# Kernel optimization log

Measured on AMD Instinct MI355X. Metric: run time of the kernel, lower is better.

## Reference

```python
import jax, jax.numpy as jnp
import numpy as np

H = 8          # num heads
DK = 64        # d_model // H
D_MODEL = 512
WIN = 256


def setup_inputs() -> dict:
    key = jax.random.key(0)
    ks = jax.random.split(key, 12)
    B, S = 2, 2048
    mk = lambda k, shape, s=1.0: jax.random.normal(k, shape, dtype=jnp.float32) * s
    inp = {
        "query": mk(ks[0], (B, S, D_MODEL)),
        "key_in": mk(ks[1], (B, S, D_MODEL)),
        "value": mk(ks[2], (B, S, D_MODEL)),
        # nn.Linear(d_model, d_model) weights (out,in) and biases, x4
        "Wq": mk(ks[3], (D_MODEL, D_MODEL), 0.02), "bq": jnp.zeros((D_MODEL,), jnp.float32),
        "Wk": mk(ks[4], (D_MODEL, D_MODEL), 0.02), "bk": jnp.zeros((D_MODEL,), jnp.float32),
        "Wv": mk(ks[5], (D_MODEL, D_MODEL), 0.02), "bv": jnp.zeros((D_MODEL,), jnp.float32),
        "Wo": mk(ks[6], (D_MODEL, D_MODEL), 0.02), "bo": jnp.zeros((D_MODEL,), jnp.float32),
    }
    return inp


def reference(query, key_in, value, Wq, bq, Wk, bk, Wv, bv, Wo, bo):
    B, S, D = query.shape
    scale = np.float32(1.0 / np.sqrt(DK))

    def proj(x, W, b):
        # (B,S,D) -> (B,H,S,DK)
        return (x @ W.T + b).reshape(B, S, H, DK).transpose(0, 2, 1, 3)

    q = proj(query, Wq, bq)
    k = proj(key_in, Wk, bk)
    v = proj(value, Wv, bv)

    # Faithful to naive_masked_matmul: full (B,H,S,S) scores, with entries
    # OUTSIDE the sliding window left at exactly 0.0 (NOT -inf) before softmax.
    scores = jnp.einsum('bhid,bhjd->bhij', q, k) * scale
    idx = jnp.arange(S)
    band = jnp.abs(idx[:, None] - idx[None, :]) <= (WIN // 2)  # (S,S) bool
    scores = jnp.where(band, scores, jnp.float32(0.0))

    p_attn = jax.nn.softmax(scores, axis=-1)
    x = jnp.einsum('bhij,bhjd->bhid', p_attn, v)          # (B,H,S,DK)
    x = x.transpose(0, 2, 1, 3).reshape(B, S, D)          # (B,S,D)
    return x @ Wo.T + bo
```

## Files before the change

kernel.cpp:

```cpp
#include <hip/hip_runtime.h>
#include <hip/hip_bf16.h>

#define SS 2048
#define DD 512
#define HWIN 128

typedef __bf16 bf16x8 __attribute__((ext_vector_type(8)));
typedef unsigned short u16x8 __attribute__((ext_vector_type(8)));
typedef float f32x4 __attribute__((ext_vector_type(4)));

__device__ __forceinline__ unsigned short f2bf(float x) {
    unsigned u = __builtin_bit_cast(unsigned, x);
    return (unsigned short)((u + 0x7fffu + ((u >> 16) & 1u)) >> 16);
}
__device__ __forceinline__ float bf2f(unsigned short s) {
    unsigned u = ((unsigned)s) << 16;
    return __builtin_bit_cast(float, u);
}
__device__ __forceinline__ void split_bf(float x, unsigned short& h, unsigned short& l) {
    h = f2bf(x);
    l = f2bf(x - bf2f(h));
}
__device__ __forceinline__ f32x4 mfma16(u16x8 a, u16x8 b, f32x4 c) {
    return __builtin_amdgcn_mfma_f32_16x16x32_bf16(
        __builtin_bit_cast(bf16x8, a), __builtin_bit_cast(bf16x8, b), c, 0, 0, 0);
}
__device__ __forceinline__ void gload16(const unsigned short* g, unsigned short* l) {
    __builtin_amdgcn_global_load_lds(
        (const __attribute__((address_space(1))) unsigned int*)g,
        (__attribute__((address_space(3))) unsigned int*)l, 16, 0, 0);
}

__global__ __launch_bounds__(256) void castAll(
    const float* __restrict__ q, const float* __restrict__ k, const float* __restrict__ v,
    const float* __restrict__ wq, const float* __restrict__ wk,
    const float* __restrict__ wv, const float* __restrict__ wo,
    unsigned short* __restrict__ QAh, unsigned short* __restrict__ KAh,
    unsigned short* __restrict__ VAh,
    unsigned short* __restrict__ WQh, unsigned short* __restrict__ WKh,
    unsigned short* __restrict__ WVh, unsigned short* __restrict__ WoP)
{
    const size_t e0 = ((size_t)blockIdx.x * 256 + threadIdx.x) * 8;
    const float* src; size_t off; unsigned short* dsth; bool paired = false;
    if      (e0 < 2097152) { src = q; off = e0;           dsth = QAh + off; }
    else if (e0 < 4194304) { src = k; off = e0 - 2097152; dsth = KAh + off; }
    else if (e0 < 6291456) { src = v; off = e0 - 4194304; dsth = VAh + off; }
    else {
        const size_t e = e0 - 6291456;
        if      (e < 262144) { src = wq; off = e;          dsth = WQh + off; }
        else if (e < 524288) { src = wk; off = e - 262144; dsth = WKh + off; }
        else if (e < 786432) { src = wv; off = e - 524288; dsth = WVh + off; }
        else { src = wo; off = e - 786432; dsth = WoP + 2 * (e - 786432); paired = true; }
    }
    const float4 f0 = *(const float4*)(src + off), f1 = *(const float4*)(src + off + 4);
    const float vals[8] = {f0.x, f0.y, f0.z, f0.w, f1.x, f1.y, f1.z, f1.w};
    u16x8 h;
    #pragma unroll
    for (int i = 0; i < 8; ++i) h[i] = f2bf(vals[i]);
    *(u16x8*)dsth = h;
    if (paired) {
        u16x8 l;
        #pragma unroll
        for (int i = 0; i < 8; ++i) l[i] = f2bf(vals[i] - bf2f(h[i]));
        *(u16x8*)(dsth + 8) = l;
    }
}

__global__ __launch_bounds__(256) void proj_gemm(
    const unsigned short* __restrict__ QAh, const unsigned short* __restrict__ KAh,
    const unsigned short* __restrict__ VAh,
    const unsigned short* __restrict__ WQh, const unsigned short* __restrict__ WKh,
    const unsigned short* __restrict__ WVh,
    const float* __restrict__ bq, const float* __restrict__ bk, const float* __restrict__ bv,
    unsigned short* __restrict__ base,
    unsigned short* __restrict__ VTH, float* __restrict__ part)
{
    const int d = blockIdx.x;
    const int hi = d >> 6, low = d & 63;
    const int x = low >> 3, rsw = low & 7;
    const int g = hi * 8 + rsw;
    const int y = g / 3, z = g - y * 3;

    const unsigned short* Ap = (z == 0) ? QAh : ((z == 1) ? KAh : VAh);
    const unsigned short* Wp = (z == 0) ? WQh : ((z == 1) ? WKh : WVh);
    const float* bias = (z == 0) ? bq : ((z == 1) ? bk : bv);
    unsigned short* OH = base + (size_t)z * 4194304;

    const int m0 = y * 128, n0 = x * 64;

    __shared__ unsigned short Ah[16 * 64 * 8];
    __shared__ unsigned short Bh[8 * 64 * 8];

    const int tid = threadIdx.x, wave = tid >> 6, lane = tid & 63;
    const int lm = lane & 15, lq = lane >> 4;
    const int wm = wave >> 1, wn = wave & 1;
    const int kb = lq * 8;

    f32x4 acc[4][2] = {};

    const int ar0 = m0 + (wave * 2 + 0) * 16 + lm;
    const int ar1 = m0 + (wave * 2 + 1) * 16 + lm;
    const int br  = n0 + wave * 16 + lm;

    const int aoff0 = ((wave * 2 + 0) * 64 + lane) * 8;
    const int aoff1 = ((wave * 2 + 1) * 64 + lane) * 8;
    const int boff  = (wave * 64 + lane) * 8;

    for (int k0 = 0; k0 < 512; k0 += 64) {
        __syncthreads();
        gload16(Ap + (size_t)ar0 * 512 + k0 + kb,      &Ah[aoff0]);
        gload16(Ap + (size_t)ar1 * 512 + k0 + kb,      &Ah[aoff1]);
        gload16(Wp + (size_t)br  * 512 + k0 + kb,      &Bh[boff]);
        gload16(Ap + (size_t)ar0 * 512 + k0 + 32 + kb, &Ah[4096 + aoff0]);
        gload16(Ap + (size_t)ar1 * 512 + k0 + 32 + kb, &Ah[4096 + aoff1]);
        gload16(Wp + (size_t)br  * 512 + k0 + 32 + kb, &Bh[2048 + boff]);
        __syncthreads();

        #pragma unroll
        for (int s = 0; s < 2; ++s) {
            u16x8 afh[4], bfh[2];
            #pragma unroll
            for (int i = 0; i < 4; ++i)
                afh[i] = *(const u16x8*)&Ah[s * 4096 + ((wm * 4 + i) * 64 + lane) * 8];
            #pragma unroll
            for (int j = 0; j < 2; ++j)
                bfh[j] = *(const u16x8*)&Bh[s * 2048 + ((wn * 2 + j) * 64 + lane) * 8];
            #pragma unroll
            for (int i = 0; i < 4; ++i)
                #pragma unroll
                for (int j = 0; j < 2; ++j)
                    acc[i][j] = mfma16(afh[i], bfh[j], acc[i][j]);
        }
    }

    if (z < 2) {
        #pragma unroll
        for (int i = 0; i < 4; ++i)
            #pragma unroll
            for (int j = 0; j < 2; ++j) {
                const int col = n0 + (wn * 2 + j) * 16 + lm;
                const float bv_ = bias[col];
                #pragma unroll
                for (int r = 0; r < 4; ++r) {
                    const int row = m0 + (wm * 4 + i) * 16 + lq * 4 + r;
                    OH[(size_t)row * 512 + col] = f2bf(acc[i][j][r] + bv_);
                }
            }
    } else {
        float csum[2] = {0.f, 0.f};
        #pragma unroll
        for (int i = 0; i < 4; ++i)
            #pragma unroll
            for (int j = 0; j < 2; ++j) {
                const int col = n0 + (wn * 2 + j) * 16 + lm;
                const float bv_ = bias[col];
                #pragma unroll
                for (int r = 0; r < 4; ++r) {
                    const int row = m0 + (wm * 4 + i) * 16 + lq * 4 + r;
                    const float vv = acc[i][j][r] + bv_;
                    csum[j] += vv;
                    const size_t vix =
                        (((size_t)(row >> 11) * 8 + (col >> 6)) * 64 + (col & 63)) * 2048
                        + (row & 2047);
                    VTH[vix] = f2bf(vv);
                }
            }
        #pragma unroll
        for (int j = 0; j < 2; ++j) {
            float s = csum[j];
            s += __shfl_xor(s, 16);
            s += __shfl_xor(s, 32);
            if (lq == 0) {
                const int col = n0 + (wn * 2 + j) * 16 + lm;
                part[(size_t)(y * 2 + wm) * 512 + col] = s;
            }
        }
    }
}

__global__ __launch_bounds__(256) void out_gemm(
    const unsigned short* __restrict__ XHg,
    const unsigned short* __restrict__ WoP, const float* __restrict__ bo,
    float* __restrict__ O)
{
    const int gid = blockIdx.x;
    const int rr = gid & 7, hi = gid >> 3;
    const int nblk = hi & 7, mhi = hi >> 3;
    const int mblk = mhi * 8 + rr;
    const int m0 = mblk * 64, n0 = nblk * 64;

    __shared__ unsigned short Ah[2 * 4096];
    __shared__ unsigned short Bh[2 * 4096], Bl[2 * 4096];

    const int tid = threadIdx.x, wave = tid >> 6, lane = tid & 63;
    const int lm = lane & 15, lq = lane >> 4;
    const int kb = lq * 8;

    f32x4 acc[4] = {};

    const int arow = m0 + wave * 16 + lm;
    const int brow = n0 + wave * 16 + lm;

    #define OSTAGE(k0_, bs)                                                     \
    {                                                                           \
        _Pragma("unroll")                                                       \
        for (int s = 0; s < 2; ++s) {                                           \
            const int o = (bs) * 4096 + ((s * 4 + wave) * 64 + lane) * 8;       \
            gload16(XHg + (size_t)arow * 512 + (k0_) + s * 32 + kb, &Ah[o]);    \
            const unsigned short* pw =                                          \
                WoP + 2 * ((size_t)brow * 512 + (k0_) + s * 32 + kb);           \
            gload16(pw,     &Bh[o]);                                            \
            gload16(pw + 8, &Bl[o]);                                            \
        }                                                                       \
    }

    OSTAGE(0, 0);
    __syncthreads();

    for (int t = 0; t < 8; ++t) {
        const int cur = t & 1;
        if (t < 7) OSTAGE((t + 1) * 64, cur ^ 1);

        #pragma unroll
        for (int s = 0; s < 2; ++s) {
            const u16x8 a_h = *(const u16x8*)&Ah[cur * 4096 + ((s * 4 + wave) * 64 + lane) * 8];
            #pragma unroll
            for (int j = 0; j < 4; ++j) {
                const u16x8 b_h = *(const u16x8*)&Bh[cur * 4096 + ((s * 4 + j) * 64 + lane) * 8];
                const u16x8 b_l = *(const u16x8*)&Bl[cur * 4096 + ((s * 4 + j) * 64 + lane) * 8];
                acc[j] = mfma16(a_h, b_h, acc[j]);
                acc[j] = mfma16(a_h, b_l, acc[j]);
            }
        }

        __syncthreads();
    }
    #undef OSTAGE

    #pragma unroll
    for (int j = 0; j < 4; ++j) {
        const int col = n0 + j * 16 + lm;
        const float bv_ = bo[col];
        #pragma unroll
        for (int r = 0; r < 4; ++r) {
            const int row = m0 + wave * 16 + lq * 4 + r;
            O[(size_t)row * 512 + col] = acc[j][r] + bv_;
        }
    }
}

__global__ __launch_bounds__(256) void attn_mfma(
    const unsigned short* __restrict__ QH, const unsigned short* __restrict__ KH,
    const unsigned short* __restrict__ VTH, const float* __restrict__ part,
    unsigned short* __restrict__ XH)
{
    const int dblk = blockIdx.x;
    const int bhi = dblk >> 8, blow = dblk & 255;
    const int xblk = blow >> 3, rrs = blow & 7;
    const int bh = bhi * 8 + rrs;
    const int h = bh & 7, b = bh >> 3;
    const int i0 = xblk * 64;
    const int tid = threadIdx.x, wave = tid >> 6, lane = tid & 63;
    const int lm = lane & 15, lq = lane >> 4;
    const int kb = lq * 8;

    __shared__ unsigned short KfH[2 * 8 * 64 * 8];
    __shared__ unsigned short VfH[2 * 8 * 64 * 8];
    __shared__ unsigned short Swh[64][72];

    const size_t qoff = ((size_t)(b * SS + i0 + wave * 16 + lm)) * DD + h * 64 + kb;
    const u16x8 aQ0h = *(const u16x8*)(QH + qoff);
    const u16x8 aQ1h = *(const u16x8*)(QH + qoff + 32);

    f32x4 oacc[4] = {};
    float dacc[4] = {0.f, 0.f, 0.f, 0.f};

    const size_t vrow = ((size_t)bh * 64 + wave * 16 + lm) * 2048;
    const int s0 = (wave * 2 + 0) * 64 * 8 + lane * 8;
    const int s1 = (wave * 2 + 1) * 64 * 8 + lane * 8;

    #define STAGE(jt_, bufsel)                                                  \
    {                                                                           \
        const int jt0_ = i0 - 128 + (jt_) * 64;                                 \
        const int jrow = jt0_ + wave * 16 + lm;                                 \
        const int jrc = min(max(jrow, 0), SS - 1);                              \
        const size_t kgb = ((size_t)(b * SS + jrc)) * DD + h * 64 + kb;         \
        gload16(KH + kgb,      &KfH[(bufsel) * 4096 + s0]);                     \
        gload16(KH + kgb + 32, &KfH[(bufsel) * 4096 + s1]);                     \
        const int j0c = min(max(jt0_ + kb, 0), SS - 8);                         \
        const int j1c = min(max(jt0_ + 32 + kb, 0), SS - 8);                    \
        gload16(VTH + vrow + j0c, &VfH[(bufsel) * 4096 + s0]);                  \
        gload16(VTH + vrow + j1c, &VfH[(bufsel) * 4096 + s1]);                  \
    }

    STAGE(0, 0);
    __syncthreads();

    for (int jt = 0; jt < 5; ++jt) {
        const int buf = jt & 1;
        if (jt < 4) STAGE(jt + 1, buf ^ 1);
        const int jt0 = i0 - 128 + jt * 64;
        const int rmin = i0 + wave * 16;

        #pragma unroll
        for (int js = 0; js < 4; ++js) {
            const int j0 = js * 16;
            const int cmin = jt0 + j0, cmax = cmin + 15;
            const bool skip = (cmax < 0) || (cmin >= SS) ||
                              (cmax < rmin - HWIN) || (cmin > rmin + 15 + HWIN);
            if (skip) {
                #pragma unroll
                for (int r = 0; r < 4; ++r)
                    Swh[wave * 16 + lq * 4 + r][j0 + lm] = 0;
                continue;
            }
            const u16x8 bK0h = *(const u16x8*)&KfH[buf * 4096 + ((js * 2 + 0) * 64 + lane) * 8];
            const u16x8 bK1h = *(const u16x8*)&KfH[buf * 4096 + ((js * 2 + 1) * 64 + lane) * 8];
            f32x4 s = {0.f, 0.f, 0.f, 0.f};
            s = mfma16(aQ0h, bK0h, s);
            s = mfma16(aQ1h, bK1h, s);
            const int jg = jt0 + j0 + lm;
            const int iq = i0 + wave * 16 + lq * 4;
            #pragma unroll
            for (int r = 0; r < 4; ++r) {
                const int qi = iq + r;
                const bool in = ((unsigned)jg < (unsigned)SS) &&
                                ((unsigned)(jg - qi + HWIN) <= (unsigned)(2 * HWIN));
                const float w = in ? (__expf(s[r] * 0.125f) - 1.0f) : 0.0f;
                dacc[r] += w;
                Swh[wave * 16 + lq * 4 + r][j0 + lm] = f2bf(w);
            }
        }

        const u16x8 aP0h = *(const u16x8*)&Swh[wave * 16 + lm][kb];
        const u16x8 aP1h = *(const u16x8*)&Swh[wave * 16 + lm][kb + 32];
        #pragma unroll
        for (int s4 = 0; s4 < 4; ++s4) {
            const u16x8 bV0h = *(const u16x8*)&VfH[buf * 4096 + ((s4 * 2 + 0) * 64 + lane) * 8];
            const u16x8 bV1h = *(const u16x8*)&VfH[buf * 4096 + ((s4 * 2 + 1) * 64 + lane) * 8];
            oacc[s4] = mfma16(aP0h, bV0h, oacc[s4]);
            oacc[s4] = mfma16(aP1h, bV1h, oacc[s4]);
        }
        __syncthreads();
    }
    #undef STAGE

    #pragma unroll
    for (int r = 0; r < 4; ++r) {
        float v = dacc[r];
        v += __shfl_xor(v, 1);
        v += __shfl_xor(v, 2);
        v += __shfl_xor(v, 4);
        v += __shfl_xor(v, 8);
        dacc[r] = v + 2048.0f;
    }

    #pragma unroll
    for (int s4 = 0; s4 < 4; ++s4) {
        const float* pp = part + (size_t)(b * 32) * 512 + h * 64 + s4 * 16 + lm;
        float vsv = 0.f;
        #pragma unroll 8
        for (int p = 0; p < 32; ++p) vsv += pp[(size_t)p * 512];
        #pragma unroll
        for (int r = 0; r < 4; ++r) {
            const int qrow = i0 + wave * 16 + lq * 4 + r;
            const float x = (oacc[s4][r] + vsv) / dacc[r];
            const size_t ix = ((size_t)(b * SS + qrow)) * DD + h * 64 + s4 * 16 + lm;
            XH[ix] = f2bf(x);
        }
    }
}

extern "C" void kernel_launch(void* const* d_in, const int* in_sizes, int n_in,
                              void* d_out, int out_size, void* d_ws, size_t ws_size,
                              hipStream_t stream)
{
    const float* query  = (const float*)d_in[0];
    const float* key_in = (const float*)d_in[1];
    const float* value  = (const float*)d_in[2];
    const float* Wq = (const float*)d_in[3]; const float* bq = (const float*)d_in[4];
    const float* Wk = (const float*)d_in[5]; const float* bk = (const float*)d_in[6];
    const float* Wv = (const float*)d_in[7]; const float* bv = (const float*)d_in[8];
    const float* Wo = (const float*)d_in[9]; const float* bo = (const float*)d_in[10];

    unsigned short* wsb = (unsigned short*)d_ws;
    unsigned short* QH  = wsb;
    unsigned short* KH  = wsb + 4194304;
    unsigned short* VTH = wsb + 8388608;
    unsigned short* XH  = wsb + 12582912;
    unsigned short* WQh = wsb + 16777216;
    unsigned short* WKh = wsb + 17039360;
    unsigned short* WVh = wsb + 17301504;
    unsigned short* WoP = wsb + 17825792;
    unsigned short* QAh = wsb + 18350080;
    unsigned short* KAh = wsb + 20447232;
    unsigned short* VAh = wsb + 22544384;
    float* partp = (float*)((char*)d_ws + 63045632);

    castAll<<<3584, 256, 0, stream>>>(query, key_in, value, Wq, Wk, Wv, Wo,
                                      QAh, KAh, VAh, WQh, WKh, WVh, WoP);

    proj_gemm<<<768, 256, 0, stream>>>(QAh, KAh, VAh, WQh, WKh, WVh,
                                       bq, bk, bv, QH, VTH, partp);

    attn_mfma<<<512, 256, 0, stream>>>(QH, KH, VTH, partp, XH);

    out_gemm<<<512, 256, 0, stream>>>(XH, WoP, bo, (float*)d_out);
}
```

Before: 144.9 us.

## Give each wave private LDS staging to drop block barriers in projection and attention

Both the QKV projection GEMM and the windowed attention kernel now have each wave load its own fragments into a per-wave LDS region and wait with s_waitcnt vmcnt(0), instead of cooperatively staging shared tiles between __syncthreads. This removes block-wide barriers and, in attention, the double-buffered prefetch. The cost is redundant global/L2 traffic, since waves reload the same B and K/V tiles, plus more LDS per block and no overlap of loads with compute. Keeping the Swh writes and reads consistent within a wave without the barrier relies on per-wave row ownership.

```diff
diff --git a/kernel.cpp b/kernel.cpp
--- a/kernel.cpp
+++ b/kernel.cpp
@@ -8,6 +8,8 @@
 typedef __bf16 bf16x8 __attribute__((ext_vector_type(8)));
 typedef unsigned short u16x8 __attribute__((ext_vector_type(8)));
 typedef float f32x4 __attribute__((ext_vector_type(4)));
+
+#define VMCNT0() asm volatile("s_waitcnt vmcnt(0)" ::: "memory")
 
 __device__ __forceinline__ unsigned short f2bf(float x) {
     unsigned u = __builtin_bit_cast(unsigned, x);
@@ -88,8 +90,8 @@
 
     const int m0 = y * 128, n0 = x * 64;
 
-    __shared__ unsigned short Ah[16 * 64 * 8];
-    __shared__ unsigned short Bh[8 * 64 * 8];
+    __shared__ unsigned short Aw[4][8][512];
+    __shared__ unsigned short Bw[4][4][512];
 
     const int tid = threadIdx.x, wave = tid >> 6, lane = tid & 63;
     const int lm = lane & 15, lq = lane >> 4;
@@ -98,33 +100,35 @@
 
     f32x4 acc[4][2] = {};
 
-    const int ar0 = m0 + (wave * 2 + 0) * 16 + lm;
-    const int ar1 = m0 + (wave * 2 + 1) * 16 + lm;
-    const int br  = n0 + wave * 16 + lm;
-
-    const int aoff0 = ((wave * 2 + 0) * 64 + lane) * 8;
-    const int aoff1 = ((wave * 2 + 1) * 64 + lane) * 8;
-    const int boff  = (wave * 64 + lane) * 8;
+    size_t arow[4], brow[2];
+    #pragma unroll
+    for (int i = 0; i < 4; ++i)
+        arow[i] = (size_t)(m0 + (wm * 4 + i) * 16 + lm) * 512;
+    #pragma unroll
+    for (int j = 0; j < 2; ++j)
+        brow[j] = (size_t)(n0 + (wn * 2 + j) * 16 + lm) * 512;
 
     for (int k0 = 0; k0 < 512; k0 += 64) {
-        __syncthreads();
-        gload16(Ap + (size_t)ar0 * 512 + k0 + kb,      &Ah[aoff0]);
-        gload16(Ap + (size_t)ar1 * 512 + k0 + kb,      &Ah[aoff1]);
-        gload16(Wp + (size_t)br  * 512 + k0 + kb,      &Bh[boff]);
-        gload16(Ap + (size_t)ar0 * 512 + k0 + 32 + kb, &Ah[4096 + aoff0]);
-        gload16(Ap + (size_t)ar1 * 512 + k0 + 32 + kb, &Ah[4096 + aoff1]);
-        gload16(Wp + (size_t)br  * 512 + k0 + 32 + kb, &Bh[2048 + boff]);
-        __syncthreads();
+        #pragma unroll
+        for (int s = 0; s < 2; ++s) {
+            #pragma unroll
+            for (int i = 0; i < 4; ++i)
+                gload16(Ap + arow[i] + k0 + s * 32 + kb, &Aw[wave][s * 4 + i][lane * 8]);
+            #pragma unroll
+            for (int j = 0; j < 2; ++j)
+                gload16(Wp + brow[j] + k0 + s * 32 + kb, &Bw[wave][s * 2 + j][lane * 8]);
+        }
+        VMCNT0();
 
         #pragma unroll
         for (int s = 0; s < 2; ++s) {
             u16x8 afh[4], bfh[2];
             #pragma unroll
             for (int i = 0; i < 4; ++i)
-                afh[i] = *(const u16x8*)&Ah[s * 4096 + ((wm * 4 + i) * 64 + lane) * 8];
+                afh[i] = *(const u16x8*)&Aw[wave][s * 4 + i][lane * 8];
             #pragma unroll
             for (int j = 0; j < 2; ++j)
-                bfh[j] = *(const u16x8*)&Bh[s * 2048 + ((wn * 2 + j) * 64 + lane) * 8];
+                bfh[j] = *(const u16x8*)&Bw[wave][s * 2 + j][lane * 8];
             #pragma unroll
             for (int i = 0; i < 4; ++i)
                 #pragma unroll
@@ -264,8 +268,8 @@
     const int lm = lane & 15, lq = lane >> 4;
     const int kb = lq * 8;
 
-    __shared__ unsigned short KfH[2 * 8 * 64 * 8];
-    __shared__ unsigned short VfH[2 * 8 * 64 * 8];
+    __shared__ unsigned short Kw[4][8][512];
+    __shared__ unsigned short Vw[4][8][512];
     __shared__ unsigned short Swh[64][72];
 
     const size_t qoff = ((size_t)(b * SS + i0 + wave * 16 + lm)) * DD + h * 64 + kb;
@@ -275,31 +279,27 @@
     f32x4 oacc[4] = {};
     float dacc[4] = {0.f, 0.f, 0.f, 0.f};
 
-    const size_t vrow = ((size_t)bh * 64 + wave * 16 + lm) * 2048;
-    const int s0 = (wave * 2 + 0) * 64 * 8 + lane * 8;
-    const int s1 = (wave * 2 + 1) * 64 * 8 + lane * 8;
-
-    #define STAGE(jt_, bufsel)                                                  \
-    {                                                                           \
-        const int jt0_ = i0 - 128 + (jt_) * 64;                                 \
-        const int jrow = jt0_ + wave * 16 + lm;                                 \
-        const int jrc = min(max(jrow, 0), SS - 1);                              \
-        const size_t kgb = ((size_t)(b * SS + jrc)) * DD + h * 64 + kb;         \
-        gload16(KH + kgb,      &KfH[(bufsel) * 4096 + s0]);                     \
-        gload16(KH + kgb + 32, &KfH[(bufsel) * 4096 + s1]);                     \
-        const int j0c = min(max(jt0_ + kb, 0), SS - 8);                         \
-        const int j1c = min(max(jt0_ + 32 + kb, 0), SS - 8);                    \
-        gload16(VTH + vrow + j0c, &VfH[(bufsel) * 4096 + s0]);                  \
-        gload16(VTH + vrow + j1c, &VfH[(bufsel) * 4096 + s1]);                  \
-    }
-
-    STAGE(0, 0);
-    __syncthreads();
-
     for (int jt = 0; jt < 5; ++jt) {
-        const int buf = jt & 1;
-        if (jt < 4) STAGE(jt + 1, buf ^ 1);
         const int jt0 = i0 - 128 + jt * 64;
+
+        #pragma unroll
+        for (int js = 0; js < 4; ++js) {
+            const int jrow = jt0 + js * 16 + lm;
+            const int jrc = min(max(jrow, 0), SS - 1);
+            const size_t kgb = ((size_t)(b * SS + jrc)) * DD + h * 64 + kb;
+            gload16(KH + kgb,      &Kw[wave][js * 2 + 0][lane * 8]);
+            gload16(KH + kgb + 32, &Kw[wave][js * 2 + 1][lane * 8]);
+        }
+        const int j0c = min(max(jt0 + kb, 0), SS - 8);
+        const int j1c = min(max(jt0 + 32 + kb, 0), SS - 8);
+        #pragma unroll
+        for (int d2 = 0; d2 < 4; ++d2) {
+            const size_t vr = ((size_t)(bh * 64 + d2 * 16 + lm)) * 2048;
+            gload16(VTH + vr + j0c, &Vw[wave][d2 * 2 + 0][lane * 8]);
+            gload16(VTH + vr + j1c, &Vw[wave][d2 * 2 + 1][lane * 8]);
+        }
+        VMCNT0();
+
         const int rmin = i0 + wave * 16;
 
         #pragma unroll
@@ -314,8 +314,8 @@
                     Swh[wave * 16 + lq * 4 + r][j0 + lm] = 0;
                 continue;
             }
-            const u16x8 bK0h = *(const u16x8*)&KfH[buf * 4096 + ((js * 2 + 0) * 64 + lane) * 8];
-            const u16x8 bK1h = *(const u16x8*)&KfH[buf * 4096 + ((js * 2 + 1) * 64 + lane) * 8];
+            const u16x8 bK0h = *(const u16x8*)&Kw[wave][js * 2 + 0][lane * 8];
+            const u16x8 bK1h = *(const u16x8*)&Kw[wave][js * 2 + 1][lane * 8];
             f32x4 s = {0.f, 0.f, 0.f, 0.f};
             s = mfma16(aQ0h, bK0h, s);
             s = mfma16(aQ1h, bK1h, s);
@@ -336,14 +336,12 @@
         const u16x8 aP1h = *(const u16x8*)&Swh[wave * 16 + lm][kb + 32];
         #pragma unroll
         for (int s4 = 0; s4 < 4; ++s4) {
-            const u16x8 bV0h = *(const u16x8*)&VfH[buf * 4096 + ((s4 * 2 + 0) * 64 + lane) * 8];
-            const u16x8 bV1h = *(const u16x8*)&VfH[buf * 4096 + ((s4 * 2 + 1) * 64 + lane) * 8];
+            const u16x8 bV0h = *(const u16x8*)&Vw[wave][s4 * 2 + 0][lane * 8];
+            const u16x8 bV1h = *(const u16x8*)&Vw[wave][s4 * 2 + 1][lane * 8];
             oacc[s4] = mfma16(aP0h, bV0h, oacc[s4]);
             oacc[s4] = mfma16(aP1h, bV1h, oacc[s4]);
         }
-        __syncthreads();
-    }
-    #undef STAGE
+    }
 
     #pragma unroll
     for (int r = 0; r < 4; ++r) {
```

After: 166.9 us. 15.2% more time.

## Double-buffer LDS tiles in QKV projection GEMM to overlap loads with MFMA

Applied to the files above, without the earlier changes.

Converts the projection GEMM's K-loop to a two-stage LDS double buffer. The next 64-wide K slice is prefetched with direct global-to-LDS loads while MFMAs run on the current slice, using manual vmcnt waits and raw barriers. This aims to hide global load latency in the projection kernel, at the cost of twice the LDS footprint (possibly lower occupancy). It also relies on the vmcnt(6) count matching the six loads issued per stage.

```diff
diff --git a/kernel.cpp b/kernel.cpp
--- a/kernel.cpp
+++ b/kernel.cpp
@@ -8,6 +8,10 @@
 typedef __bf16 bf16x8 __attribute__((ext_vector_type(8)));
 typedef unsigned short u16x8 __attribute__((ext_vector_type(8)));
 typedef float f32x4 __attribute__((ext_vector_type(4)));
+
+#define VMCNT0() asm volatile("s_waitcnt vmcnt(0)" ::: "memory")
+#define VMCNT6() asm volatile("s_waitcnt vmcnt(6)" ::: "memory")
+#define BARRIER() __builtin_amdgcn_s_barrier()
 
 __device__ __forceinline__ unsigned short f2bf(float x) {
     unsigned u = __builtin_bit_cast(unsigned, x);
@@ -88,8 +92,8 @@
 
     const int m0 = y * 128, n0 = x * 64;
 
-    __shared__ unsigned short Ah[16 * 64 * 8];
-    __shared__ unsigned short Bh[8 * 64 * 8];
+    __shared__ unsigned short Ah[2 * 8192];
+    __shared__ unsigned short Bh[2 * 4096];
 
     const int tid = threadIdx.x, wave = tid >> 6, lane = tid & 63;
     const int lm = lane & 15, lq = lane >> 4;
@@ -106,32 +110,49 @@
     const int aoff1 = ((wave * 2 + 1) * 64 + lane) * 8;
     const int boff  = (wave * 64 + lane) * 8;
 
-    for (int k0 = 0; k0 < 512; k0 += 64) {
-        __syncthreads();
-        gload16(Ap + (size_t)ar0 * 512 + k0 + kb,      &Ah[aoff0]);
-        gload16(Ap + (size_t)ar1 * 512 + k0 + kb,      &Ah[aoff1]);
-        gload16(Wp + (size_t)br  * 512 + k0 + kb,      &Bh[boff]);
-        gload16(Ap + (size_t)ar0 * 512 + k0 + 32 + kb, &Ah[4096 + aoff0]);
-        gload16(Ap + (size_t)ar1 * 512 + k0 + 32 + kb, &Ah[4096 + aoff1]);
-        gload16(Wp + (size_t)br  * 512 + k0 + 32 + kb, &Bh[2048 + boff]);
-        __syncthreads();
+    #define PSTAGE(k0_, bs)                                                     \
+    {                                                                           \
+        gload16(Ap + (size_t)ar0 * 512 + (k0_) + kb,      &Ah[(bs) * 8192 + aoff0]); \
+        gload16(Ap + (size_t)ar1 * 512 + (k0_) + kb,      &Ah[(bs) * 8192 + aoff1]); \
+        gload16(Wp + (size_t)br  * 512 + (k0_) + kb,      &Bh[(bs) * 4096 + boff]);  \
+        gload16(Ap + (size_t)ar0 * 512 + (k0_) + 32 + kb, &Ah[(bs) * 8192 + 4096 + aoff0]); \
+        gload16(Ap + (size_t)ar1 * 512 + (k0_) + 32 + kb, &Ah[(bs) * 8192 + 4096 + aoff1]); \
+        gload16(Wp + (size_t)br  * 512 + (k0_) + 32 + kb, &Bh[(bs) * 4096 + 2048 + boff]);  \
+    }
+
+    PSTAGE(0, 0);
+    VMCNT0();
+    BARRIER();
+
+    for (int t = 0; t < 8; ++t) {
+        const int cur = t & 1;
+        if (t < 7) {
+            PSTAGE((t + 1) * 64, cur ^ 1);
+            VMCNT6();
+        } else {
+            VMCNT0();
+        }
+        BARRIER();
 
         #pragma unroll
         for (int s = 0; s < 2; ++s) {
             u16x8 afh[4], bfh[2];
             #pragma unroll
             for (int i = 0; i < 4; ++i)
-                afh[i] = *(const u16x8*)&Ah[s * 4096 + ((wm * 4 + i) * 64 + lane) * 8];
+                afh[i] = *(const u16x8*)&Ah[cur * 8192 + s * 4096 + ((wm * 4 + i) * 64 + lane) * 8];
             #pragma unroll
             for (int j = 0; j < 2; ++j)
-                bfh[j] = *(const u16x8*)&Bh[s * 2048 + ((wn * 2 + j) * 64 + lane) * 8];
+                bfh[j] = *(const u16x8*)&Bh[cur * 4096 + s * 2048 + ((wn * 2 + j) * 64 + lane) * 8];
             #pragma unroll
             for (int i = 0; i < 4; ++i)
                 #pragma unroll
                 for (int j = 0; j < 2; ++j)
                     acc[i][j] = mfma16(afh[i], bfh[j], acc[i][j]);
         }
-    }
+
+        BARRIER();
+    }
+    #undef PSTAGE
 
     if (z < 2) {
         #pragma unroll
```

After: 144.8 us. About the same (-0.1%).
